# Kernel tuning notes

Hardware: AMD Instinct MI355X
Metric: run time of the kernel (lower is better)

The kernel has to match this reference:

```python
import jax, jax.numpy as jnp
import numpy as np

N_NODES = 100000
N_EDGES = 1600000
N_GRAPHS = 64


def setup_inputs() -> dict:
    key = jax.random.key(0)
    ks = jax.random.split(key, 12)
    x = jax.random.normal(ks[0], (N_NODES, 3), dtype=jnp.float32)
    edge_index = jax.random.randint(ks[1], (2, N_EDGES), 0, N_NODES)
    edge_attr = jax.random.uniform(ks[2], (N_EDGES,), dtype=jnp.float32)
    batch = jnp.sort(jax.random.randint(ks[3], (N_NODES,), 0, N_GRAPHS))

    def glorot(k, shape):
        lim = float(np.sqrt(6.0 / (shape[0] + shape[1])))
        return jax.random.uniform(k, shape, jnp.float32, -lim, lim)

    W1 = glorot(ks[4], (3, 100));    b1 = jnp.zeros((100,), jnp.float32)
    W2 = glorot(ks[5], (100, 200));  b2 = jnp.zeros((200,), jnp.float32)
    Wl1 = glorot(ks[6], (200, 100)); bl1 = jnp.zeros((100,), jnp.float32)
    Wl2 = glorot(ks[7], (100, 1));   bl2 = jnp.zeros((1,), jnp.float32)
    return {"x": x, "edge_attr": edge_attr, "W1": W1, "b1": b1, "W2": W2,
            "b2": b2, "Wl1": Wl1, "bl1": bl1, "Wl2": Wl2, "bl2": bl2,
            "edge_index": edge_index, "batch": batch}


def gcn_conv(x, edge_index, edge_weight, W, b):
    # PyG GCNConv: linear transform, add self-loops (weight 1), symmetric
    # deg^{-1/2} normalization, scatter-add messages source->target, + bias.
    h = x @ W                                   # [N, out]
    n = h.shape[0]
    loops = jnp.arange(n)
    row = jnp.concatenate([edge_index[0], loops])   # sources
    col = jnp.concatenate([edge_index[1], loops])   # targets
    w = jnp.concatenate([edge_weight, jnp.ones((n,), edge_weight.dtype)])
    deg = jax.ops.segment_sum(w, col, num_segments=n)
    dinv = jnp.where(deg > 0, jax.lax.rsqrt(deg), jnp.zeros_like(deg))
    norm = dinv[row] * w * dinv[col]                # [E+N]
    out = jax.ops.segment_sum(norm[:, None] * h[row], col, num_segments=n)
    return out + b


def reference(x, edge_attr, W1, b1, W2, b2, Wl1, bl1, Wl2, bl2, edge_index, batch):
    h = jax.nn.silu(gcn_conv(x, edge_index, edge_attr, W1, b1))
    h = jax.nn.silu(gcn_conv(h, edge_index, edge_attr, W2, b2))
    # global_mean_pool over graphs in the batch
    sums = jax.ops.segment_sum(h, batch, num_segments=N_GRAPHS)
    counts = jax.ops.segment_sum(jnp.ones((h.shape[0],), h.dtype), batch,
                                 num_segments=N_GRAPHS)
    pooled = sums / jnp.maximum(counts, 1.0)[:, None]   # [G, 200]
    h = jax.nn.silu(pooled @ Wl1 + bl1)
    out = h @ Wl2 + bl2                                  # [G, 1]
    return out.squeeze()
```

## Files before the change

### kernel.cpp

```cpp
#include <hip/hip_runtime.h>

#define NN 100000
#define NE 1600000
#define NG 64
#define CAP 64
#define NPB 80
#define NBUCK 391
#define NBLK 391
#define EPB 4096
#define BCAP 4608
#define NSLOT 32

__device__ __forceinline__ float fast_div(float n, float d) {
  return n * __builtin_amdgcn_rcpf(d);
}
__device__ __forceinline__ float silu_f(float x) {
  return fast_div(x, 1.0f + __expf(-x));
}

__global__ void k_scatter(const int* __restrict__ row, const int* __restrict__ col,
                          const float* __restrict__ ew, int* __restrict__ gcnt,
                          int2* __restrict__ sorted, float* __restrict__ pooled2) {
  __shared__ int h[NBUCK];
  __shared__ int base[NBUCK];
  __shared__ int curh[NBUCK];
  int tid = threadIdx.x;
  for (int i = tid; i < NBUCK; i += 512) { h[i] = 0; curh[i] = 0; }
  for (int i = blockIdx.x * 512 + tid; i < NG * NSLOT * 200; i += NBLK * 512)
    pooled2[i] = 0.0f;
  __syncthreads();
  int s = blockIdx.x * EPB;
  for (int i = 0; i < EPB / 2048; ++i) {
    int e = s + i * 2048 + tid * 4;
    if (e + 3 < NE) {
      int4 c4 = *(const int4*)(col + e);
      atomicAdd(&h[c4.x >> 8], 1);
      atomicAdd(&h[c4.y >> 8], 1);
      atomicAdd(&h[c4.z >> 8], 1);
      atomicAdd(&h[c4.w >> 8], 1);
    } else {
      for (int j = 0; j < 4; ++j) {
        int ee = e + j;
        if (ee < NE) atomicAdd(&h[col[ee] >> 8], 1);
      }
    }
  }
  __syncthreads();
  for (int i = tid; i < NBUCK; i += 512)
    base[i] = (h[i] > 0) ? atomicAdd(&gcnt[i * 16], h[i]) : 0;
  __syncthreads();
  for (int i = 0; i < EPB / 2048; ++i) {
    int e = s + i * 2048 + tid * 4;
    if (e + 3 < NE) {
      int4 r4 = *(const int4*)(row + e);
      int4 c4 = *(const int4*)(col + e);
      float4 w4 = *(const float4*)(ew + e);
#define SC1(cc, rr, ww) { \
  int b = (cc) >> 8; \
  int p = base[b] + atomicAdd(&curh[b], 1); \
  if (p < BCAP) \
    sorted[(size_t)b * BCAP + p] = \
        make_int2((rr) | (((cc) & 255) << 17), __float_as_int(ww)); }
      SC1(c4.x, r4.x, w4.x)
      SC1(c4.y, r4.y, w4.y)
      SC1(c4.z, r4.z, w4.z)
      SC1(c4.w, r4.w, w4.w)
    } else {
      for (int j = 0; j < 4; ++j) {
        int ee = e + j;
        if (ee < NE) { SC1(col[ee], row[ee], ew[ee]) }
      }
#undef SC1
    }
  }
}

__global__ void k_group(const int* __restrict__ gcnt, const int2* __restrict__ sorted,
                        int* __restrict__ cur, int2* __restrict__ buck,
                        const float* __restrict__ x, float4* __restrict__ y4) {
  __shared__ int cnt[256];
  __shared__ float wsum[256];
  int b = blockIdx.x, tid = threadIdx.x;
  int n = min(gcnt[b * 16], BCAP);
  size_t s = (size_t)b * BCAP;
  if (tid < 256) { cnt[tid] = 0; wsum[tid] = 0.0f; }
  __syncthreads();
  for (int i = tid; i < n; i += 512) {
    int2 pk = sorted[s + i];
    int node = (pk.x >> 17) & 255;
    int rank = atomicAdd(&cnt[node], 1);
    atomicAdd(&wsum[node], __int_as_float(pk.y));
    if (rank < CAP)
      buck[(((size_t)b * 256 + node) << 6) + rank] = make_int2(pk.x & 0x1FFFF, pk.y);
  }
  __syncthreads();
  if (tid < 256) {
    int gnode = b * 256 + tid;
    if (gnode < NN) {
      cur[gnode] = cnt[tid];
      float di = rsqrtf(wsum[tid] + 1.0f);
      y4[gnode] = make_float4(di * x[3 * gnode + 0], di * x[3 * gnode + 1],
                              di * x[3 * gnode + 2], di);
    }
  }
}

__global__ void k_agg1(const int* __restrict__ cur, const int2* __restrict__ buck,
                       const float4* __restrict__ y4, float4* __restrict__ a1d) {
  int wave = threadIdx.x >> 6, lane = threadIdx.x & 63;
  int sub = lane >> 4, rank = lane & 15;
  int cbase = blockIdx.x * 16 + wave * 4;
  int c = cbase + sub;
  int cnt = min(cur[c], CAP);
  float s0 = 0.0f, s1 = 0.0f, s2 = 0.0f;
  for (int p = rank; p < cnt; p += 16) {
    int2 pk = buck[((size_t)c << 6) + p];
    float ww = __int_as_float(pk.y);
    float4 v = y4[pk.x];
    s0 += ww * v.x;
    s1 += ww * v.y;
    s2 += ww * v.z;
  }
  for (int s = 8; s; s >>= 1) {
    s0 += __shfl_down(s0, s, 16);
    s1 += __shfl_down(s1, s, 16);
    s2 += __shfl_down(s2, s, 16);
  }
  if (rank == 0) {
    float4 vc = y4[c];
    float dc = vc.w;
    a1d[c] = make_float4((s0 + vc.x) * dc, (s1 + vc.y) * dc, (s2 + vc.z) * dc, dc);
  }
}

__global__ void k_agg2r(const float4* __restrict__ a1d, const int* __restrict__ cur,
                        const int2* __restrict__ buck, const float* __restrict__ W1,
                        const float* __restrict__ b1, float* __restrict__ a2) {
  int wave = threadIdx.x >> 6;
  int lane = threadIdx.x & 63;
  int c = blockIdx.x * 4 + wave;
  if (c >= NN) return;
  int grp = lane >> 5;
  int li = lane & 31;
  bool act = li < 25;
  float4 w0, w1, w2, bb;
  if (act) {
    w0 = ((const float4*)W1)[li];
    w1 = ((const float4*)(W1 + 100))[li];
    w2 = ((const float4*)(W1 + 200))[li];
    bb = ((const float4*)b1)[li];
  }
  float4 ac = a1d[c];
  float dc = ac.w;
  float4 acc = make_float4(0.f, 0.f, 0.f, 0.f);
#define ZACC(av, cf) { \
  float m = (cf) * (av).w; \
  float vx = bb.x + (av).x * w0.x + (av).y * w1.x + (av).z * w2.x; \
  float vy = bb.y + (av).x * w0.y + (av).y * w1.y + (av).z * w2.y; \
  float vz = bb.z + (av).x * w0.z + (av).y * w1.z + (av).z * w2.z; \
  float vw = bb.w + (av).x * w0.w + (av).y * w1.w + (av).z * w2.w; \
  acc.x += m * silu_f(vx); \
  acc.y += m * silu_f(vy); \
  acc.z += m * silu_f(vz); \
  acc.w += m * silu_f(vw); }
  if (grp == 0 && act) ZACC(ac, dc)
  int cnt = min(cur[c], CAP);
  int2 pk = make_int2(0, 0);
  if (lane < cnt) pk = buck[((size_t)c << 6) + lane];
  int p = 0;
  for (; p + 4 <= cnt; p += 4) {
    int rva = __shfl(pk.x, p + grp, 64);
    float cfa = __int_as_float(__shfl(pk.y, p + grp, 64)) * dc;
    int rvb = __shfl(pk.x, p + 2 + grp, 64);
    float cfb = __int_as_float(__shfl(pk.y, p + 2 + grp, 64)) * dc;
    float4 ava = a1d[rva];
    float4 avb = a1d[rvb];
    if (act) { ZACC(ava, cfa) ZACC(avb, cfb) }
  }
  for (; p + 2 <= cnt; p += 2) {
    int rv = __shfl(pk.x, p + grp, 64);
    float cf = __int_as_float(__shfl(pk.y, p + grp, 64)) * dc;
    float4 av = a1d[rv];
    if (act) ZACC(av, cf)
  }
  if (p < cnt) {
    int rv = __shfl(pk.x, p, 64);
    float cf = __int_as_float(__shfl(pk.y, p, 64)) * dc;
    float4 av = a1d[rv];
    if (grp == 0 && act) ZACC(av, cf)
  }
#undef ZACC
  acc.x += __shfl(acc.x, lane + 32, 64);
  acc.y += __shfl(acc.y, lane + 32, 64);
  acc.z += __shfl(acc.z, lane + 32, 64);
  acc.w += __shfl(acc.w, lane + 32, 64);
  if (grp == 0 && act) ((float4*)a2)[(size_t)c * 25 + li] = acc;
}

__global__ void k_h2pool(const float* __restrict__ a2, const float* __restrict__ W2,
                         const float* __restrict__ b2, const int* __restrict__ batch,
                         float* __restrict__ pooled2) {
  __shared__ float zst[100 * 84];
  __shared__ float part[6 * 200];
  __shared__ int bsm[NPB];
  int tid = threadIdx.x;
  int nb = blockIdx.x * NPB;
  int slot = blockIdx.x & (NSLOT - 1);
  const float4* a2v = (const float4*)(a2 + (size_t)nb * 100);
  for (int i = tid; i < NPB * 25; i += 256) {
    int n = i / 25, c = i % 25;
    float4 v = a2v[i];
    zst[(4 * c + 0) * 84 + n] = v.x;
    zst[(4 * c + 1) * 84 + n] = v.y;
    zst[(4 * c + 2) * 84 + n] = v.z;
    zst[(4 * c + 3) * 84 + n] = v.w;
  }
  if (tid < NPB) bsm[tid] = batch[nb + tid];
  for (int i = tid; i < 1200; i += 256) part[i] = 0.0f;
  __syncthreads();
  int gmin = bsm[0];
  int ngr = bsm[NPB - 1] - gmin + 1;
  int q = tid % 25;
  int r = tid / 25;
  if (r < 10) {
    int n0 = r * 8;
    float4 acc0[8], acc1[8];
#pragma unroll
    for (int i = 0; i < 8; ++i) {
      acc0[i] = make_float4(0.f, 0.f, 0.f, 0.f);
      acc1[i] = make_float4(0.f, 0.f, 0.f, 0.f);
    }
    const float4* W2v = (const float4*)W2;
#pragma unroll 2
    for (int k = 0; k < 100; ++k) {
      float4 w0 = W2v[k * 50 + 2 * q];
      float4 w1 = W2v[k * 50 + 2 * q + 1];
      float4 za = *(const float4*)&zst[k * 84 + n0];
      float4 zb = *(const float4*)&zst[k * 84 + n0 + 4];
#define FMA8(ai, zv) \
  acc0[ai].x += (zv) * w0.x; acc0[ai].y += (zv) * w0.y; \
  acc0[ai].z += (zv) * w0.z; acc0[ai].w += (zv) * w0.w; \
  acc1[ai].x += (zv) * w1.x; acc1[ai].y += (zv) * w1.y; \
  acc1[ai].z += (zv) * w1.z; acc1[ai].w += (zv) * w1.w;
      FMA8(0, za.x) FMA8(1, za.y) FMA8(2, za.z) FMA8(3, za.w)
      FMA8(4, zb.x) FMA8(5, zb.y) FMA8(6, zb.z) FMA8(7, zb.w)
#undef FMA8
    }
    float4 b0v = ((const float4*)b2)[2 * q];
    float4 b1v = ((const float4*)b2)[2 * q + 1];
    float4 run0 = make_float4(0.f, 0.f, 0.f, 0.f);
    float4 run1 = make_float4(0.f, 0.f, 0.f, 0.f);
    int curg = bsm[n0];
#define FLUSH(gv) { \
  int gl = (gv) - gmin; \
  if (gl < 6) { \
    float* pr = &part[gl * 200 + 8 * q]; \
    atomicAdd(&pr[0], run0.x); atomicAdd(&pr[1], run0.y); \
    atomicAdd(&pr[2], run0.z); atomicAdd(&pr[3], run0.w); \
    atomicAdd(&pr[4], run1.x); atomicAdd(&pr[5], run1.y); \
    atomicAdd(&pr[6], run1.z); atomicAdd(&pr[7], run1.w); \
  } else { \
    float* pr = &pooled2[((size_t)(gv) * NSLOT + slot) * 200 + 8 * q]; \
    atomicAdd(&pr[0], run0.x); atomicAdd(&pr[1], run0.y); \
    atomicAdd(&pr[2], run0.z); atomicAdd(&pr[3], run0.w); \
    atomicAdd(&pr[4], run1.x); atomicAdd(&pr[5], run1.y); \
    atomicAdd(&pr[6], run1.z); atomicAdd(&pr[7], run1.w); \
  } }
#pragma unroll
    for (int i = 0; i < 8; ++i) {
      float4 s0, s1;
      s0.x = silu_f(acc0[i].x + b0v.x); s0.y = silu_f(acc0[i].y + b0v.y);
      s0.z = silu_f(acc0[i].z + b0v.z); s0.w = silu_f(acc0[i].w + b0v.w);
      s1.x = silu_f(acc1[i].x + b1v.x); s1.y = silu_f(acc1[i].y + b1v.y);
      s1.z = silu_f(acc1[i].z + b1v.z); s1.w = silu_f(acc1[i].w + b1v.w);
      int g = bsm[n0 + i];
      if (g != curg) {
        FLUSH(curg)
        run0 = make_float4(0.f, 0.f, 0.f, 0.f);
        run1 = make_float4(0.f, 0.f, 0.f, 0.f);
        curg = g;
      }
      run0.x += s0.x; run0.y += s0.y; run0.z += s0.z; run0.w += s0.w;
      run1.x += s1.x; run1.y += s1.y; run1.z += s1.z; run1.w += s1.w;
    }
    FLUSH(curg)
#undef FLUSH
  }
  __syncthreads();
  if (tid < 200) {
    int nloop = min(ngr, 6);
    for (int g = 0; g < nloop; ++g)
      pooled2[((size_t)(gmin + g) * NSLOT + slot) * 200 + tid] = part[g * 200 + tid];
  }
}

__global__ void k_final(const float* __restrict__ pooled2, const int* __restrict__ batch,
                        const float* __restrict__ Wl1, const float* __restrict__ bl1,
                        const float* __restrict__ Wl2, const float* __restrict__ bl2,
                        float* __restrict__ out) {
  __shared__ float pm[200];
  __shared__ float hid[100];
  __shared__ int bounds[2];
  int g = blockIdx.x;
  int j = threadIdx.x;
  if (j < 2) {
    int target = g + j;
    int lo = 0, hi = NN;
    while (lo < hi) {
      int mid = (lo + hi) >> 1;
      if (batch[mid] < target) lo = mid + 1; else hi = mid;
    }
    bounds[j] = lo;
  }
  float acc = 0.0f;
  if (j < 200) {
    const float* base = pooled2 + (size_t)g * NSLOT * 200 + j;
    for (int s = 0; s < NSLOT; ++s) acc += base[s * 200];
  }
  __syncthreads();
  int cntg = bounds[1] - bounds[0];
  float inv = 1.0f / (float)((cntg > 0) ? cntg : 1);
  if (j < 200) pm[j] = acc * inv;
  __syncthreads();
  if (j < 100) {
    float a = bl1[j];
    for (int k = 0; k < 200; ++k) a += pm[k] * Wl1[k * 100 + j];
    a = silu_f(a);
    hid[j] = a * Wl2[j];
  }
  __syncthreads();
  if (j == 0) {
    float sum = bl2[0];
    for (int k = 0; k < 100; ++k) sum += hid[k];
    out[g] = sum;
  }
}

extern "C" void kernel_launch(void* const* d_in, const int* in_sizes, int n_in,
                              void* d_out, int out_size, void* d_ws, size_t ws_size,
                              hipStream_t stream) {
  const float* x   = (const float*)d_in[0];
  const float* ew  = (const float*)d_in[1];
  const float* W1  = (const float*)d_in[2];
  const float* b1  = (const float*)d_in[3];
  const float* W2  = (const float*)d_in[4];
  const float* b2  = (const float*)d_in[5];
  const float* Wl1 = (const float*)d_in[6];
  const float* bl1 = (const float*)d_in[7];
  const float* Wl2 = (const float*)d_in[8];
  const float* bl2 = (const float*)d_in[9];
  const int* ei    = (const int*)d_in[10];
  const int* batch = (const int*)d_in[11];
  const int* rowp = ei;
  const int* colp = ei + NE;
  float* out = (float*)d_out;

  char* w = (char*)d_ws;
  size_t o = 0;
  auto alloc = [&](size_t bytes) {
    char* p = w + o;
    o = (o + bytes + 255) & ~(size_t)255;
    return p;
  };
  int*    cur     = (int*)alloc((size_t)NN * 4);
  float4* y4      = (float4*)alloc((size_t)NN * 16);
  float4* a1d     = (float4*)alloc((size_t)NN * 16);
  float*  pooled2 = (float*)alloc((size_t)NG * NSLOT * 200 * 4);
  float*  a2      = (float*)alloc((size_t)NN * 100 * 4);
  int2*   buck    = (int2*)alloc((size_t)NN * CAP * 8);
  int2*   sorted  = (int2*)alloc((size_t)NBUCK * BCAP * 8);
  int*    gcnt    = (int*)alloc((size_t)NBUCK * 16 * 4);

  hipMemsetAsync(gcnt, 0, (size_t)NBUCK * 16 * 4, stream);

  k_scatter<<<NBLK, 512, 0, stream>>>(rowp, colp, ew, gcnt, sorted, pooled2);
  k_group<<<NBUCK, 512, 0, stream>>>(gcnt, sorted, cur, buck, x, y4);
  k_agg1<<<NN / 16, 256, 0, stream>>>(cur, buck, y4, a1d);
  k_agg2r<<<(NN + 3) / 4, 256, 0, stream>>>(a1d, cur, buck, W1, b1, a2);
  k_h2pool<<<NN / NPB, 256, 0, stream>>>(a2, W2, b2, batch, pooled2);
  k_final<<<NG, 256, 0, stream>>>(pooled2, batch, Wl1, bl1, Wl2, bl2, out);
}
```

Before: 288.6 us.

## Precompute layer-1 activations per node and gather them in layer-2 aggregation

```diff
diff --git a/kernel.cpp b/kernel.cpp
--- a/kernel.cpp
+++ b/kernel.cpp
@@ -131,6 +131,106 @@
     float dc = vc.w;
     a1d[c] = make_float4((s0 + vc.x) * dc, (s1 + vc.y) * dc, (s2 + vc.z) * dc, dc);
   }
+}
+
+__global__ void k_z1(const float4* __restrict__ a1d, const float* __restrict__ W1,
+                     const float* __restrict__ b1, float4* __restrict__ h1s) {
+  int tid = threadIdx.x;
+  if (tid >= 250) return;
+  int n = blockIdx.x * 10 + tid / 25;
+  int q = tid % 25;
+  float4 w0 = ((const float4*)W1)[q];
+  float4 w1 = ((const float4*)(W1 + 100))[q];
+  float4 w2 = ((const float4*)(W1 + 200))[q];
+  float4 bb = ((const float4*)b1)[q];
+  float4 av = a1d[n];
+  float di = av.w;
+  float vx = bb.x + av.x * w0.x + av.y * w1.x + av.z * w2.x;
+  float vy = bb.y + av.x * w0.y + av.y * w1.y + av.z * w2.y;
+  float vz = bb.z + av.x * w0.z + av.y * w1.z + av.z * w2.z;
+  float vw = bb.w + av.x * w0.w + av.y * w1.w + av.z * w2.w;
+  h1s[(size_t)n * 25 + q] = make_float4(di * silu_f(vx), di * silu_f(vy),
+                                        di * silu_f(vz), di * silu_f(vw));
+}
+
+__global__ void k_agg2g(const float4* __restrict__ h1s, const float4* __restrict__ a1d,
+                        const int* __restrict__ cur, const int2* __restrict__ buck,
+                        float* __restrict__ a2) {
+  int wave = threadIdx.x >> 6;
+  int lane = threadIdx.x & 63;
+  int c = blockIdx.x * 4 + wave;
+  if (c >= NN) return;
+  int grp = lane >> 5;
+  int li = lane & 31;
+  bool act = li < 25;
+  int liq = act ? li : 0;
+  float dc = ((const float*)a1d)[4 * c + 3];
+  float4 hv = h1s[(size_t)c * 25 + liq];
+  float4 acc = make_float4(0.f, 0.f, 0.f, 0.f);
+  if (grp == 0 && act) acc = hv;
+  int cnt = min(cur[c], CAP);
+  int2 pk = make_int2(0, 0);
+  if (lane < cnt) pk = buck[((size_t)c << 6) + lane];
+  int p = 0;
+  for (; p + 8 <= cnt; p += 8) {
+    int r0 = __shfl(pk.x, p + grp, 64);
+    float e0 = __int_as_float(__shfl(pk.y, p + grp, 64));
+    int r1 = __shfl(pk.x, p + 2 + grp, 64);
+    float e1 = __int_as_float(__shfl(pk.y, p + 2 + grp, 64));
+    int r2 = __shfl(pk.x, p + 4 + grp, 64);
+    float e2 = __int_as_float(__shfl(pk.y, p + 4 + grp, 64));
+    int r3 = __shfl(pk.x, p + 6 + grp, 64);
+    float e3 = __int_as_float(__shfl(pk.y, p + 6 + grp, 64));
+    float4 v0 = h1s[(size_t)r0 * 25 + liq];
+    float4 v1 = h1s[(size_t)r1 * 25 + liq];
+    float4 v2 = h1s[(size_t)r2 * 25 + liq];
+    float4 v3 = h1s[(size_t)r3 * 25 + liq];
+    if (act) {
+      acc.x += e0 * v0.x + e1 * v1.x + e2 * v2.x + e3 * v3.x;
+      acc.y += e0 * v0.y + e1 * v1.y + e2 * v2.y + e3 * v3.y;
+      acc.z += e0 * v0.z + e1 * v1.z + e2 * v2.z + e3 * v3.z;
+      acc.w += e0 * v0.w + e1 * v1.w + e2 * v2.w + e3 * v3.w;
+    }
+  }
+  for (; p + 4 <= cnt; p += 4) {
+    int r0 = __shfl(pk.x, p + grp, 64);
+    float e0 = __int_as_float(__shfl(pk.y, p + grp, 64));
+    int r1 = __shfl(pk.x, p + 2 + grp, 64);
+    float e1 = __int_as_float(__shfl(pk.y, p + 2 + grp, 64));
+    float4 v0 = h1s[(size_t)r0 * 25 + liq];
+    float4 v1 = h1s[(size_t)r1 * 25 + liq];
+    if (act) {
+      acc.x += e0 * v0.x + e1 * v1.x;
+      acc.y += e0 * v0.y + e1 * v1.y;
+      acc.z += e0 * v0.z + e1 * v1.z;
+      acc.w += e0 * v0.w + e1 * v1.w;
+    }
+  }
+  for (; p + 2 <= cnt; p += 2) {
+    int r0 = __shfl(pk.x, p + grp, 64);
+    float e0 = __int_as_float(__shfl(pk.y, p + grp, 64));
+    float4 v0 = h1s[(size_t)r0 * 25 + liq];
+    if (act) {
+      acc.x += e0 * v0.x; acc.y += e0 * v0.y;
+      acc.z += e0 * v0.z; acc.w += e0 * v0.w;
+    }
+  }
+  if (p < cnt) {
+    int r0 = __shfl(pk.x, p, 64);
+    float e0 = __int_as_float(__shfl(pk.y, p, 64));
+    float4 v0 = h1s[(size_t)r0 * 25 + liq];
+    if (grp == 0 && act) {
+      acc.x += e0 * v0.x; acc.y += e0 * v0.y;
+      acc.z += e0 * v0.z; acc.w += e0 * v0.w;
+    }
+  }
+  acc.x += __shfl(acc.x, lane + 32, 64);
+  acc.y += __shfl(acc.y, lane + 32, 64);
+  acc.z += __shfl(acc.z, lane + 32, 64);
+  acc.w += __shfl(acc.w, lane + 32, 64);
+  if (grp == 0 && act)
+    ((float4*)a2)[(size_t)c * 25 + li] =
+        make_float4(dc * acc.x, dc * acc.y, dc * acc.z, dc * acc.w);
 }
 
 __global__ void k_agg2r(const float4* __restrict__ a1d, const int* __restrict__ cur,
@@ -368,15 +468,28 @@
   float*  pooled2 = (float*)alloc((size_t)NG * NSLOT * 200 * 4);
   float*  a2      = (float*)alloc((size_t)NN * 100 * 4);
   int2*   buck    = (int2*)alloc((size_t)NN * CAP * 8);
-  int2*   sorted  = (int2*)alloc((size_t)NBUCK * BCAP * 8);
-  int*    gcnt    = (int*)alloc((size_t)NBUCK * 16 * 4);
-
-  hipMemsetAsync(gcnt, 0, (size_t)NBUCK * 16 * 4, stream);
+  size_t need_sorted = (size_t)NBUCK * BCAP * 8;
+  size_t need_h1s    = (size_t)NN * 100 * 4;
+  size_t gcnt_bytes  = (size_t)NBUCK * 16 * 4;
+  size_t o_uni = o;
+  bool use_h1s =
+      (o_uni + ((need_h1s + 255) & ~(size_t)255) + gcnt_bytes + 256) <= ws_size;
+  char* uni = alloc(use_h1s ? need_h1s : need_sorted);
+  int2*   sorted = (int2*)uni;
+  float4* h1s    = (float4*)uni;
+  int*    gcnt   = (int*)alloc(gcnt_bytes);
+
+  hipMemsetAsync(gcnt, 0, gcnt_bytes, stream);
 
   k_scatter<<<NBLK, 512, 0, stream>>>(rowp, colp, ew, gcnt, sorted, pooled2);
   k_group<<<NBUCK, 512, 0, stream>>>(gcnt, sorted, cur, buck, x, y4);
   k_agg1<<<NN / 16, 256, 0, stream>>>(cur, buck, y4, a1d);
-  k_agg2r<<<(NN + 3) / 4, 256, 0, stream>>>(a1d, cur, buck, W1, b1, a2);
+  if (use_h1s) {
+    k_z1<<<NN / 10, 256, 0, stream>>>(a1d, W1, b1, h1s);
+    k_agg2g<<<(NN + 3) / 4, 256, 0, stream>>>(h1s, a1d, cur, buck, a2);
+  } else {
+    k_agg2r<<<(NN + 3) / 4, 256, 0, stream>>>(a1d, cur, buck, W1, b1, a2);
+  }
   k_h2pool<<<NN / NPB, 256, 0, stream>>>(a2, W2, b2, batch, pooled2);
   k_final<<<NG, 256, 0, stream>>>(pooled2, batch, Wl1, bl1, Wl2, bl2, out);
 }
```

Result: slower. 342.3 us (+18.6%).

## Precompute layer-1 activations once and gather them in column-chunked layout

Applied to the files above, without the earlier changes.

```diff
diff --git a/kernel.cpp b/kernel.cpp
--- a/kernel.cpp
+++ b/kernel.cpp
@@ -130,6 +130,75 @@
     float4 vc = y4[c];
     float dc = vc.w;
     a1d[c] = make_float4((s0 + vc.x) * dc, (s1 + vc.y) * dc, (s2 + vc.z) * dc, dc);
+  }
+}
+
+__global__ void k_z1(const float4* __restrict__ a1d, const float* __restrict__ W1,
+                     const float* __restrict__ b1, float4* __restrict__ h1c) {
+  int tid = threadIdx.x;
+  if (tid >= 250) return;
+  int n = blockIdx.x * 10 + tid / 25;
+  int qq = tid % 25;
+  float4 w0 = ((const float4*)W1)[qq];
+  float4 w1 = ((const float4*)(W1 + 100))[qq];
+  float4 w2 = ((const float4*)(W1 + 200))[qq];
+  float4 bb = ((const float4*)b1)[qq];
+  float4 av = a1d[n];
+  float di = av.w;
+  float vx = bb.x + av.x * w0.x + av.y * w1.x + av.z * w2.x;
+  float vy = bb.y + av.x * w0.y + av.y * w1.y + av.z * w2.y;
+  float vz = bb.z + av.x * w0.z + av.y * w1.z + av.z * w2.z;
+  float vw = bb.w + av.x * w0.w + av.y * w1.w + av.z * w2.w;
+  h1c[(size_t)(qq / 5) * (NN * 5) + (size_t)n * 5 + (qq % 5)] =
+      make_float4(di * silu_f(vx), di * silu_f(vy), di * silu_f(vz),
+                  di * silu_f(vw));
+}
+
+__global__ void k_agg2c(const float4* __restrict__ h1c, const float4* __restrict__ a1d,
+                        const int* __restrict__ cur, const int2* __restrict__ buck,
+                        float* __restrict__ a2) {
+  int wave = threadIdx.x >> 6, lane = threadIdx.x & 63;
+  int bq = blockIdx.x / 25000;
+  int c  = (blockIdx.x % 25000) * 4 + wave;
+  int e8 = lane >> 3, qd = lane & 7;
+  int qdq = (qd < 5) ? qd : 0;
+  const float4* tab = h1c + (size_t)bq * (NN * 5);
+  int cnt = min(cur[c], CAP);
+  int2 pk = make_int2(0, 0);
+  if (lane < cnt) pk = buck[((size_t)c << 6) + lane];
+  float4 acc = make_float4(0.f, 0.f, 0.f, 0.f);
+#define RND4(P0) { \
+  int r0 = __shfl(pk.x, (P0) + e8, 64); \
+  float w0 = __int_as_float(__shfl(pk.y, (P0) + e8, 64)); \
+  int r1 = __shfl(pk.x, (P0) + 8 + e8, 64); \
+  float w1 = __int_as_float(__shfl(pk.y, (P0) + 8 + e8, 64)); \
+  int r2 = __shfl(pk.x, (P0) + 16 + e8, 64); \
+  float w2 = __int_as_float(__shfl(pk.y, (P0) + 16 + e8, 64)); \
+  int r3 = __shfl(pk.x, (P0) + 24 + e8, 64); \
+  float w3 = __int_as_float(__shfl(pk.y, (P0) + 24 + e8, 64)); \
+  float4 v0 = tab[(size_t)r0 * 5 + qdq]; \
+  float4 v1 = tab[(size_t)r1 * 5 + qdq]; \
+  float4 v2 = tab[(size_t)r2 * 5 + qdq]; \
+  float4 v3 = tab[(size_t)r3 * 5 + qdq]; \
+  acc.x += w0 * v0.x + w1 * v1.x + w2 * v2.x + w3 * v3.x; \
+  acc.y += w0 * v0.y + w1 * v1.y + w2 * v2.y + w3 * v3.y; \
+  acc.z += w0 * v0.z + w1 * v1.z + w2 * v2.z + w3 * v3.z; \
+  acc.w += w0 * v0.w + w1 * v1.w + w2 * v2.w + w3 * v3.w; }
+  RND4(0)
+  if (cnt > 32) RND4(32)
+#undef RND4
+  acc.x += __shfl_down(acc.x, 32); acc.y += __shfl_down(acc.y, 32);
+  acc.z += __shfl_down(acc.z, 32); acc.w += __shfl_down(acc.w, 32);
+  acc.x += __shfl_down(acc.x, 16); acc.y += __shfl_down(acc.y, 16);
+  acc.z += __shfl_down(acc.z, 16); acc.w += __shfl_down(acc.w, 16);
+  acc.x += __shfl_down(acc.x, 8);  acc.y += __shfl_down(acc.y, 8);
+  acc.z += __shfl_down(acc.z, 8);  acc.w += __shfl_down(acc.w, 8);
+  if (lane < 5) {
+    float4 sv = tab[(size_t)c * 5 + lane];
+    float dc = ((const float*)a1d)[4 * c + 3];
+    ((float4*)a2)[(size_t)c * 25 + bq * 5 + lane] =
+        make_float4(dc * (acc.x + sv.x), dc * (acc.y + sv.y),
+                    dc * (acc.z + sv.z), dc * (acc.w + sv.w));
   }
 }
 
@@ -368,15 +437,28 @@
   float*  pooled2 = (float*)alloc((size_t)NG * NSLOT * 200 * 4);
   float*  a2      = (float*)alloc((size_t)NN * 100 * 4);
   int2*   buck    = (int2*)alloc((size_t)NN * CAP * 8);
-  int2*   sorted  = (int2*)alloc((size_t)NBUCK * BCAP * 8);
-  int*    gcnt    = (int*)alloc((size_t)NBUCK * 16 * 4);
-
-  hipMemsetAsync(gcnt, 0, (size_t)NBUCK * 16 * 4, stream);
+  size_t need_sorted = (size_t)NBUCK * BCAP * 8;
+  size_t need_h1c    = (size_t)NN * 100 * 4;
+  size_t gcnt_bytes  = (size_t)NBUCK * 16 * 4;
+  size_t o_uni = o;
+  bool use_h1c =
+      (o_uni + ((need_h1c + 255) & ~(size_t)255) + gcnt_bytes + 256) <= ws_size;
+  char* uni = alloc(use_h1c ? need_h1c : need_sorted);
+  int2*   sorted = (int2*)uni;
+  float4* h1c    = (float4*)uni;
+  int*    gcnt   = (int*)alloc(gcnt_bytes);
+
+  hipMemsetAsync(gcnt, 0, gcnt_bytes, stream);
 
   k_scatter<<<NBLK, 512, 0, stream>>>(rowp, colp, ew, gcnt, sorted, pooled2);
   k_group<<<NBUCK, 512, 0, stream>>>(gcnt, sorted, cur, buck, x, y4);
   k_agg1<<<NN / 16, 256, 0, stream>>>(cur, buck, y4, a1d);
-  k_agg2r<<<(NN + 3) / 4, 256, 0, stream>>>(a1d, cur, buck, W1, b1, a2);
+  if (use_h1c) {
+    k_z1<<<NN / 10, 256, 0, stream>>>(a1d, W1, b1, h1c);
+    k_agg2c<<<5 * (NN / 4), 256, 0, stream>>>(h1c, a1d, cur, buck, a2);
+  } else {
+    k_agg2r<<<(NN + 3) / 4, 256, 0, stream>>>(a1d, cur, buck, W1, b1, a2);
+  }
   k_h2pool<<<NN / NPB, 256, 0, stream>>>(a2, W2, b2, batch, pooled2);
   k_final<<<NG, 256, 0, stream>>>(pooled2, batch, Wl1, bl1, Wl2, bl2, out);
 }
```

Result: slower. 389.5 us (+35.0%).

## Build per-node edge buckets with global atomics and simplify layer-2 gather loop

Applied to the files above, without the earlier changes.

```diff
diff --git a/kernel.cpp b/kernel.cpp
--- a/kernel.cpp
+++ b/kernel.cpp
@@ -5,10 +5,6 @@
 #define NG 64
 #define CAP 64
 #define NPB 80
-#define NBUCK 391
-#define NBLK 391
-#define EPB 4096
-#define BCAP 4608
 #define NSLOT 32
 
 __device__ __forceinline__ float fast_div(float n, float d) {
@@ -18,91 +14,45 @@
   return fast_div(x, 1.0f + __expf(-x));
 }
 
-__global__ void k_scatter(const int* __restrict__ row, const int* __restrict__ col,
-                          const float* __restrict__ ew, int* __restrict__ gcnt,
-                          int2* __restrict__ sorted, float* __restrict__ pooled2) {
-  __shared__ int h[NBUCK];
-  __shared__ int base[NBUCK];
-  __shared__ int curh[NBUCK];
-  int tid = threadIdx.x;
-  for (int i = tid; i < NBUCK; i += 512) { h[i] = 0; curh[i] = 0; }
-  for (int i = blockIdx.x * 512 + tid; i < NG * NSLOT * 200; i += NBLK * 512)
-    pooled2[i] = 0.0f;
-  __syncthreads();
-  int s = blockIdx.x * EPB;
-  for (int i = 0; i < EPB / 2048; ++i) {
-    int e = s + i * 2048 + tid * 4;
-    if (e + 3 < NE) {
-      int4 c4 = *(const int4*)(col + e);
-      atomicAdd(&h[c4.x >> 8], 1);
-      atomicAdd(&h[c4.y >> 8], 1);
-      atomicAdd(&h[c4.z >> 8], 1);
-      atomicAdd(&h[c4.w >> 8], 1);
-    } else {
-      for (int j = 0; j < 4; ++j) {
-        int ee = e + j;
-        if (ee < NE) atomicAdd(&h[col[ee] >> 8], 1);
-      }
-    }
-  }
-  __syncthreads();
-  for (int i = tid; i < NBUCK; i += 512)
-    base[i] = (h[i] > 0) ? atomicAdd(&gcnt[i * 16], h[i]) : 0;
-  __syncthreads();
-  for (int i = 0; i < EPB / 2048; ++i) {
-    int e = s + i * 2048 + tid * 4;
-    if (e + 3 < NE) {
-      int4 r4 = *(const int4*)(row + e);
-      int4 c4 = *(const int4*)(col + e);
-      float4 w4 = *(const float4*)(ew + e);
-#define SC1(cc, rr, ww) { \
-  int b = (cc) >> 8; \
-  int p = base[b] + atomicAdd(&curh[b], 1); \
-  if (p < BCAP) \
-    sorted[(size_t)b * BCAP + p] = \
-        make_int2((rr) | (((cc) & 255) << 17), __float_as_int(ww)); }
-      SC1(c4.x, r4.x, w4.x)
-      SC1(c4.y, r4.y, w4.y)
-      SC1(c4.z, r4.z, w4.z)
-      SC1(c4.w, r4.w, w4.w)
-    } else {
-      for (int j = 0; j < 4; ++j) {
-        int ee = e + j;
-        if (ee < NE) { SC1(col[ee], row[ee], ew[ee]) }
-      }
-#undef SC1
-    }
-  }
-}
-
-__global__ void k_group(const int* __restrict__ gcnt, const int2* __restrict__ sorted,
-                        int* __restrict__ cur, int2* __restrict__ buck,
-                        const float* __restrict__ x, float4* __restrict__ y4) {
-  __shared__ int cnt[256];
-  __shared__ float wsum[256];
-  int b = blockIdx.x, tid = threadIdx.x;
-  int n = min(gcnt[b * 16], BCAP);
-  size_t s = (size_t)b * BCAP;
-  if (tid < 256) { cnt[tid] = 0; wsum[tid] = 0.0f; }
-  __syncthreads();
-  for (int i = tid; i < n; i += 512) {
-    int2 pk = sorted[s + i];
-    int node = (pk.x >> 17) & 255;
-    int rank = atomicAdd(&cnt[node], 1);
-    atomicAdd(&wsum[node], __int_as_float(pk.y));
-    if (rank < CAP)
-      buck[(((size_t)b * 256 + node) << 6) + rank] = make_int2(pk.x & 0x1FFFF, pk.y);
-  }
-  __syncthreads();
-  if (tid < 256) {
-    int gnode = b * 256 + tid;
-    if (gnode < NN) {
-      cur[gnode] = cnt[tid];
-      float di = rsqrtf(wsum[tid] + 1.0f);
-      y4[gnode] = make_float4(di * x[3 * gnode + 0], di * x[3 * gnode + 1],
-                              di * x[3 * gnode + 2], di);
-    }
-  }
+__global__ void k_build(const int* __restrict__ row, const int* __restrict__ col,
+                        const float* __restrict__ ew, int* __restrict__ cur,
+                        int2* __restrict__ buck) {
+  int i = blockIdx.x * 256 + threadIdx.x;
+  int e = i * 4;
+#define INS(cc, rr, ww) { \
+  int rk = atomicAdd(&cur[cc], 1); \
+  if (rk < CAP) buck[((size_t)(cc) << 6) + rk] = make_int2(rr, __float_as_int(ww)); }
+  if (e + 3 < NE) {
+    int4 r4 = *(const int4*)(row + e);
+    int4 c4 = *(const int4*)(col + e);
+    float4 w4 = *(const float4*)(ew + e);
+    INS(c4.x, r4.x, w4.x)
+    INS(c4.y, r4.y, w4.y)
+    INS(c4.z, r4.z, w4.z)
+    INS(c4.w, r4.w, w4.w)
+  } else {
+    for (int j = 0; j < 4; ++j) {
+      int ee = e + j;
+      if (ee < NE) { INS(col[ee], row[ee], ew[ee]) }
+    }
+  }
+#undef INS
+}
+
+__global__ void k_y4(int* __restrict__ cur, int2* __restrict__ buck,
+                     const float* __restrict__ x, float4* __restrict__ y4) {
+  int n = blockIdx.x * 256 + threadIdx.x;
+  if (n >= NN) return;
+  int cnt = min(cur[n], CAP);
+  cur[n] = cnt;
+  size_t base = (size_t)n << 6;
+  float ws = 0.0f;
+  for (int p = 0; p < cnt; ++p) ws += __int_as_float(buck[base + p].y);
+  int pe = min((cnt + 3) & ~3, CAP);
+  for (int p = cnt; p < pe; ++p) buck[base + p] = make_int2(0, 0);
+  float di = rsqrtf(ws + 1.0f);
+  y4[n] = make_float4(di * x[3 * n + 0], di * x[3 * n + 1],
+                      di * x[3 * n + 2], di);
 }
 
 __global__ void k_agg1(const int* __restrict__ cur, const int2* __restrict__ buck,
@@ -111,7 +61,7 @@
   int sub = lane >> 4, rank = lane & 15;
   int cbase = blockIdx.x * 16 + wave * 4;
   int c = cbase + sub;
-  int cnt = min(cur[c], CAP);
+  int cnt = cur[c];
   float s0 = 0.0f, s1 = 0.0f, s2 = 0.0f;
   for (int p = rank; p < cnt; p += 16) {
     int2 pk = buck[((size_t)c << 6) + p];
@@ -133,23 +83,19 @@
   }
 }
 
-__global__ void k_agg2r(const float4* __restrict__ a1d, const int* __restrict__ cur,
+__global__ void k_agg2s(const float4* __restrict__ a1d, const int* __restrict__ cur,
                         const int2* __restrict__ buck, const float* __restrict__ W1,
                         const float* __restrict__ b1, float* __restrict__ a2) {
   int wave = threadIdx.x >> 6;
   int lane = threadIdx.x & 63;
   int c = blockIdx.x * 4 + wave;
-  if (c >= NN) return;
   int grp = lane >> 5;
   int li = lane & 31;
-  bool act = li < 25;
-  float4 w0, w1, w2, bb;
-  if (act) {
-    w0 = ((const float4*)W1)[li];
-    w1 = ((const float4*)(W1 + 100))[li];
-    w2 = ((const float4*)(W1 + 200))[li];
-    bb = ((const float4*)b1)[li];
-  }
+  int liq = (li < 25) ? li : 24;
+  float4 w0 = ((const float4*)W1)[liq];
+  float4 w1 = ((const float4*)(W1 + 100))[liq];
+  float4 w2 = ((const float4*)(W1 + 200))[liq];
+  float4 bb = ((const float4*)b1)[liq];
   float4 ac = a1d[c];
   float dc = ac.w;
   float4 acc = make_float4(0.f, 0.f, 0.f, 0.f);
@@ -163,38 +109,24 @@
   acc.y += m * silu_f(vy); \
   acc.z += m * silu_f(vz); \
   acc.w += m * silu_f(vw); }
-  if (grp == 0 && act) ZACC(ac, dc)
-  int cnt = min(cur[c], CAP);
-  int2 pk = make_int2(0, 0);
-  if (lane < cnt) pk = buck[((size_t)c << 6) + lane];
-  int p = 0;
-  for (; p + 4 <= cnt; p += 4) {
-    int rva = __shfl(pk.x, p + grp, 64);
-    float cfa = __int_as_float(__shfl(pk.y, p + grp, 64)) * dc;
-    int rvb = __shfl(pk.x, p + 2 + grp, 64);
-    float cfb = __int_as_float(__shfl(pk.y, p + 2 + grp, 64)) * dc;
-    float4 ava = a1d[rva];
-    float4 avb = a1d[rvb];
-    if (act) { ZACC(ava, cfa) ZACC(avb, cfb) }
-  }
-  for (; p + 2 <= cnt; p += 2) {
-    int rv = __shfl(pk.x, p + grp, 64);
-    float cf = __int_as_float(__shfl(pk.y, p + grp, 64)) * dc;
-    float4 av = a1d[rv];
-    if (act) ZACC(av, cf)
-  }
-  if (p < cnt) {
-    int rv = __shfl(pk.x, p, 64);
-    float cf = __int_as_float(__shfl(pk.y, p, 64)) * dc;
-    float4 av = a1d[rv];
-    if (grp == 0 && act) ZACC(av, cf)
+  if (grp == 0) ZACC(ac, dc)
+  int cnt = cur[c];
+  const int2* eb = buck + ((size_t)c << 6);
+  for (int p = 0; p < cnt; p += 4) {
+    int4 ee = *(const int4*)(eb + p + 2 * grp);
+    float4 av0 = a1d[ee.x];
+    float4 av1 = a1d[ee.z];
+    float cf0 = __int_as_float(ee.y) * dc;
+    float cf1 = __int_as_float(ee.w) * dc;
+    ZACC(av0, cf0)
+    ZACC(av1, cf1)
   }
 #undef ZACC
   acc.x += __shfl(acc.x, lane + 32, 64);
   acc.y += __shfl(acc.y, lane + 32, 64);
   acc.z += __shfl(acc.z, lane + 32, 64);
   acc.w += __shfl(acc.w, lane + 32, 64);
-  if (grp == 0 && act) ((float4*)a2)[(size_t)c * 25 + li] = acc;
+  if (grp == 0 && li < 25) ((float4*)a2)[(size_t)c * 25 + li] = acc;
 }
 
 __global__ void k_h2pool(const float* __restrict__ a2, const float* __restrict__ W2,
@@ -368,15 +300,14 @@
   float*  pooled2 = (float*)alloc((size_t)NG * NSLOT * 200 * 4);
   float*  a2      = (float*)alloc((size_t)NN * 100 * 4);
   int2*   buck    = (int2*)alloc((size_t)NN * CAP * 8);
-  int2*   sorted  = (int2*)alloc((size_t)NBUCK * BCAP * 8);
-  int*    gcnt    = (int*)alloc((size_t)NBUCK * 16 * 4);
-
-  hipMemsetAsync(gcnt, 0, (size_t)NBUCK * 16 * 4, stream);
-
-  k_scatter<<<NBLK, 512, 0, stream>>>(rowp, colp, ew, gcnt, sorted, pooled2);
-  k_group<<<NBUCK, 512, 0, stream>>>(gcnt, sorted, cur, buck, x, y4);
+
+  hipMemsetAsync(cur, 0, (size_t)NN * 4, stream);
+  hipMemsetAsync(pooled2, 0, (size_t)NG * NSLOT * 200 * 4, stream);
+
+  k_build<<<(NE / 4 + 255) / 256, 256, 0, stream>>>(rowp, colp, ew, cur, buck);
+  k_y4<<<(NN + 255) / 256, 256, 0, stream>>>(cur, buck, x, y4);
   k_agg1<<<NN / 16, 256, 0, stream>>>(cur, buck, y4, a1d);
-  k_agg2r<<<(NN + 3) / 4, 256, 0, stream>>>(a1d, cur, buck, W1, b1, a2);
+  k_agg2s<<<NN / 4, 256, 0, stream>>>(a1d, cur, buck, W1, b1, a2);
   k_h2pool<<<NN / NPB, 256, 0, stream>>>(a2, W2, b2, batch, pooled2);
   k_final<<<NG, 256, 0, stream>>>(pooled2, batch, Wl1, bl1, Wl2, bl2, out);
 }
```

New measurement: 403.0 us. 39.7% more time.
